# Optimization experiments

Measured on AMD Instinct MI355X. Metric: run time of the kernel, lower is better.

## Reference

```python
import jax, jax.numpy as jnp
import numpy as np

Q = 128      # number of slices
S = 8        # slice_length = C // Q = 1024 // 128
H = 32       # unit_dim[0]
BN_EPS = 1e-3  # Keras BatchNormalization default epsilon


def setup_inputs() -> dict:
    key = jax.random.key(0)
    ks = jax.random.split(key, 5)
    B = 32768
    x = jax.random.normal(ks[0], (B, 1, 1, Q * S), dtype=jnp.float32)
    # Per-slice (grouped) parameters for the q=128 independent MLPs.
    W1 = jax.random.normal(ks[1], (Q, S, H), dtype=jnp.float32) / np.sqrt(S)
    b1 = jnp.zeros((Q, H), dtype=jnp.float32)
    gamma = jnp.ones((Q, H), dtype=jnp.float32)
    beta = jnp.zeros((Q, H), dtype=jnp.float32)
    mov_mean = 0.1 * jax.random.normal(ks[2], (Q, H), dtype=jnp.float32)
    mov_var = jnp.ones((Q, H), dtype=jnp.float32) + 0.1 * jax.random.uniform(ks[3], (Q, H), dtype=jnp.float32)
    W2 = jax.random.normal(ks[4], (Q, H, 1), dtype=jnp.float32) / np.sqrt(H)
    b2 = jnp.zeros((Q, 1), dtype=jnp.float32)
    return {"x": x, "W1": W1, "b1": b1, "gamma": gamma, "beta": beta,
            "mov_mean": mov_mean, "mov_var": mov_var, "W2": W2, "b2": b2}


def reference(x, W1, b1, gamma, beta, mov_mean, mov_var, W2, b2):
    B = x.shape[0]
    xs = x.reshape(B, Q, -1)                       # (B, Q, S)
    # Grouped Dense(32) + ELU, all 128 slices in one batched matmul
    h = jnp.einsum('bqs,qsh->bqh', xs, W1) + b1    # (B, Q, H)
    h = jax.nn.elu(h)
    # BatchNormalization (inference: moving statistics)
    inv = gamma * jax.lax.rsqrt(mov_var + BN_EPS)  # (Q, H)
    h = (h - mov_mean) * inv + beta
    # Grouped Dense(1)
    out = jnp.einsum('bqh,qho->bqo', h, W2) + b2   # (B, Q, 1)
    return out[..., 0]                              # (B, Q)
```

## Files before the change

### kernel.cpp

```cpp
#include <hip/hip_runtime.h>
#include <hip/hip_bf16.h>


#define QN 128
#define SN 8
#define HN 32
#define XROW 1024
#define BN_EPS 1e-3f
#define ROWS_BLK 128
#define CHUNK 32
#define QBLK 16

typedef short bf16x8 __attribute__((ext_vector_type(8)));
typedef float f32x16 __attribute__((ext_vector_type(16)));
typedef unsigned int u32;

typedef __attribute__((address_space(1))) void as1_void;
typedef __attribute__((address_space(3))) void as3_void;

#define WS_A_BYTES (QN * 64 * 16)
#define WS_W_OFF   WS_A_BYTES
#define WS_W_BYTES (QN * 32 * 4)
#define WS_B2_OFF  (WS_W_OFF + WS_W_BYTES)

static __device__ __forceinline__ u32 pkbf(float lo, float hi) {
    union { __hip_bfloat162 h2; u32 u; } c;
    c.h2 = __float22bfloat162_rn(float2{lo, hi});
    return c.u;
}

__global__ void divenc_prep(const float* __restrict__ W1, const float* __restrict__ b1,
                            const float* __restrict__ gamma_, const float* __restrict__ beta_,
                            const float* __restrict__ mmean, const float* __restrict__ mvar,
                            const float* __restrict__ W2, const float* __restrict__ b2,
                            unsigned char* __restrict__ ws)
{
    const int q = blockIdx.x;
    const int m = threadIdx.x;

    u32 d0 = 0, d1 = 0, d2 = 0, d3 = 0;
    if (m < 32) {
        d0 = pkbf(W1[(q*SN + 0)*HN + m], W1[(q*SN + 1)*HN + m]);
        d1 = pkbf(W1[(q*SN + 2)*HN + m], W1[(q*SN + 3)*HN + m]);
        d2 = pkbf(W1[(q*SN + 4)*HN + m], W1[(q*SN + 5)*HN + m]);
        d3 = pkbf(W1[(q*SN + 6)*HN + m], W1[(q*SN + 7)*HN + m]);
    } else {
        d0 = pkbf(b1[q*HN + (m - 32)], 0.f);
    }
    ((uint4*)ws)[q*64 + m] = uint4{d0, d1, d2, d3};

    float* wsW  = (float*)(ws + WS_W_OFF);
    float* wsB2 = (float*)(ws + WS_B2_OFF);
    if (m < 32) {
        const int half = m >> 4, r = m & 15;
        const int h = (r & 3) + 8*(r >> 2) + 4*half;
        float inv = gamma_[q*HN+h] * rsqrtf(mvar[q*HN+h] + BN_EPS);
        wsW[q*32 + m] = inv * W2[q*HN + h];
    }
    if (m == 0) {
        float acc = b2[q];
        for (int h = 0; h < HN; ++h) {
            float inv = gamma_[q*HN+h] * rsqrtf(mvar[q*HN+h] + BN_EPS);
            float w2p = inv * W2[q*HN + h];
            acc += (beta_[q*HN+h] - mmean[q*HN+h]*inv) * W2[q*HN+h] - w2p;
        }
        wsB2[q] = acc;
    }
}

__device__ __forceinline__
void stage_chunk(const float* __restrict__ x, u32* buf,
                 int b0, int q0, int c, int wv, int lane)
{
    #pragma unroll
    for (int k = 0; k < 2; ++k) {
        const int i  = wv * 2 + k;
        const int r  = i * 2 + (lane >> 5);
        const int jl = (lane & 31) ^ r;
        const float* src = x + (size_t)(b0 + c * CHUNK + r) * XROW + q0 * SN + jl * 4;
        u32* dst = buf + i * 256;
        __builtin_amdgcn_global_load_lds((const as1_void*)src, (as3_void*)dst, 16, 0, 0);
    }
}

__global__ __launch_bounds__(512, 8)
void divenc_mfma(const float* __restrict__ x, const unsigned char* __restrict__ ws,
                 float* __restrict__ out)
{
    const int tid  = threadIdx.x;
    const int lane = tid & 63;
    const int wv   = tid >> 6;
    const int half = lane >> 5;
    const int bl   = lane & 31;
    const bool hi  = lane >= 32;
    const int b0   = blockIdx.x * ROWS_BLK;
    const int q0   = blockIdx.y * QBLK;

    const uint4* wsA  = (const uint4*)ws;
    const float* wsW  = (const float*)(ws + WS_W_OFF);
    const float* wsB2 = (const float*)(ws + WS_B2_OFF);

    __shared__ u32   xbuf[2][CHUNK * 128];
    __shared__ float slab[ROWS_BLK][QBLK + 1];

    stage_chunk(x, xbuf[0], b0, q0, 0, wv, lane);

    #pragma unroll 1
    for (int c = 0; c < 4; ++c) {
        __syncthreads();

        if (c < 3) stage_chunk(x, xbuf[(c + 1) & 1], b0, q0, c + 1, wv, lane);

        const u32* xb = xbuf[c & 1];

        #pragma unroll
        for (int qg = 0; qg < 2; ++qg) {
            const int qloc = qg * 8 + wv;
            const int q    = q0 + qloc;

            union { uint4 u; bf16x8 v; } A;
            A.u = wsA[q * 64 + lane];

            float w2r[16];
            const float* wp_ = wsW + q * 32 + half * 16;
            #pragma unroll
            for (int r = 0; r < 16; ++r) w2r[r] = wp_[r];
            const float b2p = wsB2[q];

            const u32* rowp = xb + bl * 128;
            const uint4 xw0 = *(const uint4*)(rowp + (((2 * qloc)     ^ bl) * 4));
            const uint4 xw1 = *(const uint4*)(rowp + (((2 * qloc + 1) ^ bl) * 4));

            union { uint4 u; bf16x8 v; } B;
            B.u = uint4{
                hi ? 0x00003F80u : pkbf(__uint_as_float(xw0.x), __uint_as_float(xw0.y)),
                hi ? 0u          : pkbf(__uint_as_float(xw0.z), __uint_as_float(xw0.w)),
                hi ? 0u          : pkbf(__uint_as_float(xw1.x), __uint_as_float(xw1.y)),
                hi ? 0u          : pkbf(__uint_as_float(xw1.z), __uint_as_float(xw1.w)) };

            const f32x16 Z = {0.f,0.f,0.f,0.f,0.f,0.f,0.f,0.f,
                              0.f,0.f,0.f,0.f,0.f,0.f,0.f,0.f};
            f32x16 D = __builtin_amdgcn_mfma_f32_32x32x16_bf16(A.v, B.v, Z, 0, 0, 0);

            float p0 = 0.f, p1 = 0.f;
            #pragma unroll
            for (int r = 0; r < 16; ++r) {
                const float z = D[r];
                const float E = __expf(fminf(z, 0.f));
                const float R = fmaxf(z, 0.f);
                p0 = fmaf(E, w2r[r], p0);
                p1 = fmaf(R, w2r[r], p1);
            }
            float p = p0 + p1;
            p += __shfl_xor(p, 32);
            if (!hi) slab[c * CHUNK + bl][qloc] = p + b2p;
        }
    }

    __syncthreads();

    {
        const int row = tid >> 2;
        const int c4  = (tid & 3) * 4;
        float4 vv;
        vv.x = slab[row][c4 + 0];
        vv.y = slab[row][c4 + 1];
        vv.z = slab[row][c4 + 2];
        vv.w = slab[row][c4 + 3];
        *(float4*)(out + (size_t)(b0 + row) * QN + q0 + c4) = vv;
    }
}

extern "C" void kernel_launch(void* const* d_in, const int* in_sizes, int n_in,
                              void* d_out, int out_size, void* d_ws, size_t ws_size,
                              hipStream_t stream) {
    const float* x      = (const float*)d_in[0];
    const float* W1     = (const float*)d_in[1];
    const float* b1     = (const float*)d_in[2];
    const float* gamma_ = (const float*)d_in[3];
    const float* beta_  = (const float*)d_in[4];
    const float* mmean  = (const float*)d_in[5];
    const float* mvar   = (const float*)d_in[6];
    const float* W2     = (const float*)d_in[7];
    const float* b2     = (const float*)d_in[8];
    float* out = (float*)d_out;
    unsigned char* ws = (unsigned char*)d_ws;

    const int Btot = in_sizes[0] / XROW;

    divenc_prep<<<QN, 64, 0, stream>>>(W1, b1, gamma_, beta_, mmean, mvar, W2, b2, ws);
    divenc_mfma<<<dim3(Btot / ROWS_BLK, QN / QBLK), 512, 0, stream>>>(x, ws, out);
}
```

Baseline: 53.63 us.

## Stage weights into LDS and use explicit vmcnt waits for x prefetch

Per-block weights (A fragments, folded W2, b2) are now async-copied into LDS with global_load_lds, and the compute loop reads them from LDS instead of global memory. The __syncthreads is replaced with manual s_barrier plus s_waitcnt vmcnt(2), so the next chunk's loads can stay in flight while only the current chunk is awaited. This removes repeated global weight loads per wave and tightens the double-buffer pipeline. The occupancy hint in launch_bounds drops from 8 to 4, and correctness depends on the hand-written vmcnt counting matching the number of outstanding loads.

After: 58.21 us. +8.5%, slower.

```diff
diff --git a/kernel.cpp b/kernel.cpp
--- a/kernel.cpp
+++ b/kernel.cpp
@@ -22,6 +22,14 @@
 #define WS_W_OFF   WS_A_BYTES
 #define WS_W_BYTES (QN * 32 * 4)
 #define WS_B2_OFF  (WS_W_OFF + WS_W_BYTES)
+
+#define XB0   0
+#define XB1   4096
+#define LWA   8192
+#define LWW   12288
+#define LB2   12800
+#define LSLAB 12816
+#define LDS_U32 (12816 + 128*17)
 
 static __device__ __forceinline__ u32 pkbf(float lo, float hi) {
     union { __hip_bfloat162 h2; u32 u; } c;
@@ -83,7 +91,7 @@
     }
 }
 
-__global__ __launch_bounds__(512, 8)
+__global__ __launch_bounds__(512, 4)
 void divenc_mfma(const float* __restrict__ x, const unsigned char* __restrict__ ws,
                  float* __restrict__ out)
 {
@@ -96,36 +104,53 @@
     const int b0   = blockIdx.x * ROWS_BLK;
     const int q0   = blockIdx.y * QBLK;
 
-    const uint4* wsA  = (const uint4*)ws;
-    const float* wsW  = (const float*)(ws + WS_W_OFF);
-    const float* wsB2 = (const float*)(ws + WS_B2_OFF);
-
-    __shared__ u32   xbuf[2][CHUNK * 128];
-    __shared__ float slab[ROWS_BLK][QBLK + 1];
-
-    stage_chunk(x, xbuf[0], b0, q0, 0, wv, lane);
+    __shared__ __align__(16) u32 smem[LDS_U32];
+
+    #pragma unroll
+    for (int k = 0; k < 2; ++k) {
+        const int j = wv * 2 + k;
+        const unsigned char* src = ws + (size_t)(q0 + j) * 1024 + lane * 16;
+        __builtin_amdgcn_global_load_lds((const as1_void*)src,
+                                         (as3_void*)(smem + LWA + j * 256), 16, 0, 0);
+    }
+    if (wv == 0 || wv == 1) {
+        const unsigned char* src = ws + WS_W_OFF + (size_t)q0 * 128 + wv * 1024 + lane * 16;
+        __builtin_amdgcn_global_load_lds((const as1_void*)src,
+                                         (as3_void*)(smem + LWW + wv * 256), 16, 0, 0);
+    }
+    if (wv == 2 && lane < 16) {
+        const unsigned char* src = ws + WS_B2_OFF + (size_t)q0 * 4 + lane * 4;
+        __builtin_amdgcn_global_load_lds((const as1_void*)src,
+                                         (as3_void*)(smem + LB2), 4, 0, 0);
+    }
+    stage_chunk(x, smem + XB0, b0, q0, 0, wv, lane);
 
     #pragma unroll 1
     for (int c = 0; c < 4; ++c) {
-        __syncthreads();
-
-        if (c < 3) stage_chunk(x, xbuf[(c + 1) & 1], b0, q0, c + 1, wv, lane);
-
-        const u32* xb = xbuf[c & 1];
+        asm volatile("s_barrier" ::: "memory");
+        if (c < 3) {
+            stage_chunk(x, smem + (((c + 1) & 1) ? XB1 : XB0), b0, q0, c + 1, wv, lane);
+            asm volatile("s_waitcnt vmcnt(2)" ::: "memory");
+        } else {
+            asm volatile("s_waitcnt vmcnt(0)" ::: "memory");
+        }
+        asm volatile("s_barrier" ::: "memory");
+        __builtin_amdgcn_sched_barrier(0);
+
+        const u32* xb = smem + ((c & 1) ? XB1 : XB0);
 
         #pragma unroll
         for (int qg = 0; qg < 2; ++qg) {
             const int qloc = qg * 8 + wv;
-            const int q    = q0 + qloc;
 
             union { uint4 u; bf16x8 v; } A;
-            A.u = wsA[q * 64 + lane];
+            A.u = *(const uint4*)(smem + LWA + qloc * 256 + lane * 4);
 
             float w2r[16];
-            const float* wp_ = wsW + q * 32 + half * 16;
+            const float* wrp = (const float*)(smem + LWW) + qloc * 32 + half * 16;
             #pragma unroll
-            for (int r = 0; r < 16; ++r) w2r[r] = wp_[r];
-            const float b2p = wsB2[q];
+            for (int r = 0; r < 16; ++r) w2r[r] = wrp[r];
+            const float b2p = ((const float*)(smem + LB2))[qloc];
 
             const u32* rowp = xb + bl * 128;
             const uint4 xw0 = *(const uint4*)(rowp + (((2 * qloc)     ^ bl) * 4));
@@ -153,7 +178,7 @@
             }
             float p = p0 + p1;
             p += __shfl_xor(p, 32);
-            if (!hi) slab[c * CHUNK + bl][qloc] = p + b2p;
+            if (!hi) ((float*)(smem + LSLAB))[(c * CHUNK + bl) * 17 + qloc] = p + b2p;
         }
     }
 
@@ -162,11 +187,9 @@
     {
         const int row = tid >> 2;
         const int c4  = (tid & 3) * 4;
+        const float* srow = (const float*)(smem + LSLAB) + row * 17 + c4;
         float4 vv;
-        vv.x = slab[row][c4 + 0];
-        vv.y = slab[row][c4 + 1];
-        vv.z = slab[row][c4 + 2];
-        vv.w = slab[row][c4 + 3];
+        vv.x = srow[0]; vv.y = srow[1]; vv.z = srow[2]; vv.w = srow[3];
         *(float4*)(out + (size_t)(b0 + row) * QN + q0 + c4) = vv;
     }
 }
```
